# Kernel tuning notes

Hardware: AMD Instinct MI355X
Metric: run time of the kernel (lower is better)

The kernel has to match this reference:

```python
import jax, jax.numpy as jnp
import numpy as np

B, N, C = 4, 2048, 1024
H = 16
D = C // H
FF = 4096
EPS = 1e-6


def _layernorm(x, g, b):
    mu = jnp.mean(x, axis=-1, keepdims=True)
    var = jnp.mean(jnp.square(x - mu), axis=-1, keepdims=True)
    return (x - mu) * jax.lax.rsqrt(var + EPS) * g + b


def setup_inputs() -> dict:
    key = jax.random.key(0)
    ks = jax.random.split(key, 8)
    s = 0.02
    x = jax.random.normal(ks[0], (B, N, C), dtype=jnp.float32)
    mask = jnp.tril(jnp.ones((N, N), dtype=bool))[None, None]  # causal [1,1,N,N]
    return {
        "x": x,
        "mask": mask,
        "qkv_w": jax.random.normal(ks[1], (3 * C, C), jnp.float32) * s,
        "qkv_b": jnp.zeros((3 * C,), jnp.float32),
        "proj_w": jax.random.normal(ks[2], (C, C), jnp.float32) * s,
        "proj_b": jnp.zeros((C,), jnp.float32),
        "ln1_g": jnp.ones((C,), jnp.float32),
        "ln1_b": jnp.zeros((C,), jnp.float32),
        "ln2_g": jnp.ones((C,), jnp.float32),
        "ln2_b": jnp.zeros((C,), jnp.float32),
        "w1": jax.random.normal(ks[3], (FF, C), jnp.float32) * s,
        "w2": jax.random.normal(ks[4], (C, FF), jnp.float32) * s,
        "w3": jax.random.normal(ks[5], (FF, C), jnp.float32) * s,
    }


def reference(x, mask, qkv_w, qkv_b, proj_w, proj_b, ln1_g, ln1_b, ln2_g, ln2_b, w1, w2, w3):
    # --- attention sub-block (pre-norm) ---
    h = _layernorm(x, ln1_g, ln1_b)
    qkv = h @ qkv_w.T + qkv_b                      # [B,N,3C]
    qkv = qkv.reshape(B, N, 3, H, D).transpose(2, 0, 3, 1, 4)  # [3,B,H,N,D]
    q, k, v = qkv[0], qkv[1], qkv[2]
    scale = D ** -0.5
    attn = jnp.einsum("bhnd,bhmd->bhnm", q, k) * scale
    attn = jnp.where(mask, attn, -jnp.inf)
    attn = jax.nn.softmax(attn, axis=-1)
    o = jnp.einsum("bhnm,bhmd->bhnd", attn, v)
    o = o.transpose(0, 2, 1, 3).reshape(B, N, C)
    o = o @ proj_w.T + proj_b
    x = x + o  # dropout is identity in eval mode
    # --- SwiGLU MLP sub-block (pre-norm) ---
    h = _layernorm(x, ln2_g, ln2_b)
    m = (jax.nn.silu(h @ w1.T) * (h @ w3.T)) @ w2.T
    return x + m
```

## Files before the change

kernel.cpp:

```cpp
#include <hip/hip_runtime.h>
#include <hip/hip_bf16.h>
#include <stdint.h>

#define NB   4
#define NSEQ 2048
#define NC   1024
#define NH   16
#define ND   64
#define NFF  4096
#define NM   (NB*NSEQ)

typedef __attribute__((ext_vector_type(8))) short short8v;
typedef __attribute__((ext_vector_type(4))) short short4v;
typedef __attribute__((ext_vector_type(4))) float f32x4;

#define GPTR(p) ((const __attribute__((address_space(1))) void*)(p))
#define LPTR(p) ((__attribute__((address_space(3))) void*)(p))

__device__ __forceinline__ short f2bf(float f){
  unsigned u = __builtin_bit_cast(unsigned, f);
  u += 0x7fffu + ((u >> 16) & 1u);
  return (short)(u >> 16);
}
__device__ __forceinline__ float bf2f(short h){
  unsigned u = ((unsigned)(unsigned short)h) << 16;
  return __builtin_bit_cast(float, u);
}
__device__ __forceinline__ f32x4 mfma16x32(short8v a, short8v b, f32x4 c){
  return __builtin_amdgcn_mfma_f32_16x16x32_bf16(a, b, c, 0, 0, 0);
}
__device__ __forceinline__ f32x4 mfma16x16(short4v a, short4v b, f32x4 c){
  return __builtin_amdgcn_mfma_f32_16x16x16bf16_1k(a, b, c, 0, 0, 0);
}
__device__ __forceinline__ short4v pack4bf(f32x4 v){
  __hip_bfloat162 a = __float22bfloat162_rn(float2{v[0], v[1]});
  __hip_bfloat162 b = __float22bfloat162_rn(float2{v[2], v[3]});
  short4v r;
  __builtin_memcpy(&r, &a, 4);
  __builtin_memcpy(((char*)&r) + 4, &b, 4);
  return r;
}

__device__ __forceinline__ int xcd_swizzle(){
  int nwg = gridDim.x * gridDim.y;
  int wg  = blockIdx.y * gridDim.x + blockIdx.x;
  return (wg & 7) * (nwg >> 3) + (wg >> 3);
}

__global__ __launch_bounds__(256) void cvt_kernel(const float* __restrict__ w,
                                                  short* __restrict__ o, int n){
  int i = (blockIdx.x * 256 + threadIdx.x) * 4;
  if (i >= n) return;
  float4 v = *(const float4*)(w + i);
  short4v r = { f2bf(v.x), f2bf(v.y), f2bf(v.z), f2bf(v.w) };
  *(short4v*)(o + i) = r;
}

__global__ __launch_bounds__(256) void ln_kernel(const float* __restrict__ x,
                                                 const float* __restrict__ g,
                                                 const float* __restrict__ bta,
                                                 short* __restrict__ out){
  int row = blockIdx.x;
  int tid = threadIdx.x;
  int lane = tid & 63, w = tid >> 6;
  const float4* xr = (const float4*)(x + (size_t)row * NC);
  float4 v = xr[tid];
  float s1 = v.x + v.y + v.z + v.w;
  float s2 = v.x*v.x + v.y*v.y + v.z*v.z + v.w*v.w;
  #pragma unroll
  for (int off = 32; off; off >>= 1){
    s1 += __shfl_xor(s1, off);
    s2 += __shfl_xor(s2, off);
  }
  __shared__ float red[8];
  if (lane == 0){ red[w] = s1; red[4 + w] = s2; }
  __syncthreads();
  s1 = red[0] + red[1] + red[2] + red[3];
  s2 = red[4] + red[5] + red[6] + red[7];
  float mean = s1 * (1.0f / NC);
  float var  = s2 * (1.0f / NC) - mean * mean;
  float inv  = rsqrtf(var + 1e-6f);
  float4 gv = ((const float4*)g)[tid];
  float4 bv = ((const float4*)bta)[tid];
  short4v o = { f2bf((v.x - mean) * inv * gv.x + bv.x),
                f2bf((v.y - mean) * inv * gv.y + bv.y),
                f2bf((v.z - mean) * inv * gv.z + bv.z),
                f2bf((v.w - mean) * inv * gv.w + bv.w) };
  *(short4v*)(out + (size_t)row * NC + tid * 4) = o;
}

template<bool HAS_BIAS, bool HAS_RES, bool OUT_BF16, bool QKV_V>
__global__ __launch_bounds__(256, 2) void gemm_bt(const short* __restrict__ A,
                                                  const short* __restrict__ Bm,
                                                  const float* __restrict__ bias,
                                                  const float* __restrict__ res,
                                                  void* __restrict__ outp,
                                                  short* __restrict__ vt,
                                                  int Nc, int K){
  __shared__ short Al[128 * 32];
  __shared__ short Bl[128 * 32];
  int tid = threadIdx.x;
  int swz = xcd_swizzle();
  int m0 = (swz / gridDim.x) * 128, n0 = (swz % gridDim.x) * 128;
  const short* Ag = A + (size_t)m0 * K;
  const short* Bg = Bm + (size_t)n0 * K;
  int lr = tid >> 2, lc = (tid & 3) * 8;
  int lane = tid & 63, wid = tid >> 6;
  int wm = (wid >> 1) * 64, wn = (wid & 1) * 64;
  int qd = lane >> 4, l15 = lane & 15;

  f32x4 acc[4][4] = {};

  for (int k0 = 0; k0 < K; k0 += 32){
    __syncthreads();
    #pragma unroll
    for (int i = 0; i < 2; i++){
      int r = i * 64 + lr;
      __builtin_amdgcn_global_load_lds(GPTR(Ag + (size_t)r * K + k0 + lc),
                                       LPTR(&Al[r * 32 + lc]), 16, 0, 0);
      __builtin_amdgcn_global_load_lds(GPTR(Bg + (size_t)r * K + k0 + lc),
                                       LPTR(&Bl[r * 32 + lc]), 16, 0, 0);
    }
    __syncthreads();
    short8v a[4], b[4];
    #pragma unroll
    for (int t = 0; t < 4; t++)
      a[t] = *(const short8v*)&Al[(wm + t * 16 + l15) * 32 + qd * 8];
    #pragma unroll
    for (int t = 0; t < 4; t++)
      b[t] = *(const short8v*)&Bl[(wn + t * 16 + l15) * 32 + qd * 8];
    #pragma unroll
    for (int i = 0; i < 4; i++)
      #pragma unroll
      for (int j = 0; j < 4; j++)
        acc[i][j] = mfma16x32(a[i], b[j], acc[i][j]);
  }

  #pragma unroll
  for (int ti = 0; ti < 4; ti++){
    #pragma unroll
    for (int tj = 0; tj < 4; tj++){
      int col = n0 + wn + tj * 16 + l15;
      float bv = HAS_BIAS ? bias[col] : 0.0f;
      #pragma unroll
      for (int r = 0; r < 4; r++){
        int row = m0 + wm + ti * 16 + qd * 4 + r;
        float v = acc[ti][tj][r] + bv;
        if (QKV_V && col >= 2048){
          int hh = (col - 2048) >> 6, dd = col & 63;
          int bb = row >> 11, nn = row & 2047;
          vt[(((size_t)(bb * 16 + hh) * 64 + dd) << 11) + nn] = f2bf(v);
        } else {
          size_t idx = (size_t)row * Nc + col;
          if (HAS_RES) v += res[idx];
          if (OUT_BF16) ((short*)outp)[idx] = f2bf(v);
          else          ((float*)outp)[idx] = v;
        }
      }
    }
  }
}

__global__ __launch_bounds__(256, 2) void gemm_ff13(const short* __restrict__ A,
                                                    const short* __restrict__ B1m,
                                                    const short* __restrict__ B3m,
                                                    short* __restrict__ outp){
  __shared__ short Al [128 * 32];
  __shared__ short B1l[128 * 32];
  __shared__ short B3l[128 * 32];
  int tid = threadIdx.x;
  int swz = xcd_swizzle();
  int m0 = (swz / gridDim.x) * 128, n0 = (swz % gridDim.x) * 128;
  const short* Ag  = A   + (size_t)m0 * NC;
  const short* B1g = B1m + (size_t)n0 * NC;
  const short* B3g = B3m + (size_t)n0 * NC;
  int lr = tid >> 2, lc = (tid & 3) * 8;
  int lane = tid & 63, wid = tid >> 6;
  int wm = (wid >> 1) * 64, wn = (wid & 1) * 64;
  int qd = lane >> 4, l15 = lane & 15;

  f32x4 acc1[4][4] = {}, acc3[4][4] = {};

  for (int k0 = 0; k0 < NC; k0 += 32){
    __syncthreads();
    #pragma unroll
    for (int i = 0; i < 2; i++){
      int r = i * 64 + lr;
      __builtin_amdgcn_global_load_lds(GPTR(Ag + (size_t)r * NC + k0 + lc),
                                       LPTR(&Al[r * 32 + lc]), 16, 0, 0);
      __builtin_amdgcn_global_load_lds(GPTR(B1g + (size_t)r * NC + k0 + lc),
                                       LPTR(&B1l[r * 32 + lc]), 16, 0, 0);
      __builtin_amdgcn_global_load_lds(GPTR(B3g + (size_t)r * NC + k0 + lc),
                                       LPTR(&B3l[r * 32 + lc]), 16, 0, 0);
    }
    __syncthreads();
    short8v a[4], b1[4], b3[4];
    #pragma unroll
    for (int t = 0; t < 4; t++)
      a[t] = *(const short8v*)&Al[(wm + t * 16 + l15) * 32 + qd * 8];
    #pragma unroll
    for (int t = 0; t < 4; t++){
      b1[t] = *(const short8v*)&B1l[(wn + t * 16 + l15) * 32 + qd * 8];
      b3[t] = *(const short8v*)&B3l[(wn + t * 16 + l15) * 32 + qd * 8];
    }
    #pragma unroll
    for (int i = 0; i < 4; i++)
      #pragma unroll
      for (int j = 0; j < 4; j++){
        acc1[i][j] = mfma16x32(a[i], b1[j], acc1[i][j]);
        acc3[i][j] = mfma16x32(a[i], b3[j], acc3[i][j]);
      }
  }

  #pragma unroll
  for (int ti = 0; ti < 4; ti++){
    #pragma unroll
    for (int tj = 0; tj < 4; tj++){
      int col = n0 + wn + tj * 16 + l15;
      #pragma unroll
      for (int r = 0; r < 4; r++){
        int row = m0 + wm + ti * 16 + qd * 4 + r;
        float v1 = acc1[ti][tj][r];
        float v3 = acc3[ti][tj][r];
        float s = v1 / (1.0f + __expf(-v1)) * v3;
        outp[(size_t)row * NFF + col] = f2bf(s);
      }
    }
  }
}

__global__ __launch_bounds__(256) void attn_kernel(const short* __restrict__ qkvb,
                                                   const short* __restrict__ vt,
                                                   short* __restrict__ outb){
  const float QSCALE = 0.125f * 1.44269504f;
  int bh = blockIdx.x;
  int qb = 15 - blockIdx.y;
  int b = bh >> 4, h = bh & 15;
  int tid = threadIdx.x;
  int lane = tid & 63, wid = tid >> 6;
  int qd = lane >> 4, l15 = lane & 15;
  int qs = qb * 128 + wid * 32;

  const short* qbase = qkvb + (size_t)b * NSEQ * 3072 + h * 64;
  const short* kbase = qbase + 1024;
  const short* vtb   = vt + ((size_t)bh << 17);

  __shared__ short Kl[2][64 * 64];
  __shared__ short Vl[2][64 * 64];

  short8v qf[2][2];
  #pragma unroll
  for (int g = 0; g < 2; g++)
    #pragma unroll
    for (int kc = 0; kc < 2; kc++){
      short8v q = *(const short8v*)(qbase + (size_t)(qs + g * 16 + l15) * 3072
                                    + kc * 32 + qd * 8);
      short8v r;
      #pragma unroll
      for (int j = 0; j < 8; j++) r[j] = f2bf(bf2f(q[j]) * QSCALE);
      qf[g][kc] = r;
    }

  float l_i[2] = { 0.f, 0.f };
  f32x4 o[2][4];
  #pragma unroll
  for (int g = 0; g < 2; g++)
    #pragma unroll
    for (int t = 0; t < 4; t++)
      o[g][t] = (f32x4){0.f, 0.f, 0.f, 0.f};

  int nkt_blk = 2 * qb + 2;
  int itmax   = (qs + 31) >> 6;

  auto STAGE = [&](int bufi, int k0){
    #pragma unroll
    for (int i = 0; i < 2; i++){
      int cg = (wid * 2 + i) * 64 + lane;
      int r  = cg >> 3, c = cg & 7;
      int sc = (c ^ (r & 7)) << 3;
      __builtin_amdgcn_global_load_lds(GPTR(kbase + (size_t)(k0 + r) * 3072 + sc),
                                       LPTR(&Kl[bufi][cg * 8]), 16, 0, 0);
      __builtin_amdgcn_global_load_lds(GPTR(vtb + ((size_t)r << 11) + k0 + sc),
                                       LPTR(&Vl[bufi][cg * 8]), 16, 0, 0);
    }
  };

  STAGE(0, 0);
  __syncthreads();
  int cur = 0;

  for (int it = 0; it < nkt_blk; ++it){
    if (it + 1 < nkt_blk) STAGE(cur ^ 1, (it + 1) * 64);

    if (it <= itmax){
      int k0 = it * 64;
      short8v kf[4][2];
      #pragma unroll
      for (int kt = 0; kt < 4; kt++)
        #pragma unroll
        for (int kc = 0; kc < 2; kc++){
          int r = kt * 16 + l15;
          kf[kt][kc] = *(const short8v*)
              &Kl[cur][r * 64 + (((kc * 4 + qd) ^ (r & 7)) << 3)];
        }
      short4v vf[4][4];
      #pragma unroll
      for (int t = 0; t < 4; t++)
        #pragma unroll
        for (int ks = 0; ks < 4; ks++){
          int r = t * 16 + l15;
          vf[t][ks] = *(const short4v*)
              &Vl[cur][r * 64 + (((ks * 2 + (qd >> 1)) ^ (r & 7)) << 3)
                       + ((qd & 1) << 2)];
        }

      f32x4 s[2][4];
      #pragma unroll
      for (int g = 0; g < 2; g++)
        #pragma unroll
        for (int kt = 0; kt < 4; kt++){
          f32x4 z = (f32x4){0.f, 0.f, 0.f, 0.f};
          z = mfma16x32(kf[kt][0], qf[g][0], z);
          s[g][kt] = mfma16x32(kf[kt][1], qf[g][1], z);
        }

      if (it == itmax){
        #pragma unroll
        for (int g = 0; g < 2; g++){
          int qg = qs + g * 16 + l15;
          #pragma unroll
          for (int kt = 0; kt < 4; kt++)
            #pragma unroll
            for (int r = 0; r < 4; r++){
              int kg = k0 + kt * 16 + qd * 4 + r;
              s[g][kt][r] = (kg <= qg) ? s[g][kt][r] : -1e30f;
            }
        }
      }

      short4v pb[2][4];
      #pragma unroll
      for (int g = 0; g < 2; g++){
        #pragma unroll
        for (int kt = 0; kt < 4; kt++){
          f32x4 p;
          #pragma unroll
          for (int r = 0; r < 4; r++){
            float pv = exp2f(fminf(s[g][kt][r], 24.0f));
            p[r] = pv;
            l_i[g] += pv;
          }
          pb[g][kt] = pack4bf(p);
        }
      }

      #pragma unroll
      for (int g = 0; g < 2; g++)
        #pragma unroll
        for (int t = 0; t < 4; t++)
          #pragma unroll
          for (int ks = 0; ks < 4; ks++)
            o[g][t] = mfma16x16(vf[t][ks], pb[g][ks], o[g][t]);
    }

    __syncthreads();
    cur ^= 1;
  }

  #pragma unroll
  for (int g = 0; g < 2; g++){
    float l = l_i[g];
    l += __shfl_xor(l, 16);
    l += __shfl_xor(l, 32);
    float inv_l = 1.0f / l;
    int q = qs + g * 16 + l15;
    size_t rowbase = ((size_t)(b * NSEQ + q)) * NC + h * 64;
    #pragma unroll
    for (int t = 0; t < 4; t++){
      f32x4 v = { o[g][t][0] * inv_l, o[g][t][1] * inv_l,
                  o[g][t][2] * inv_l, o[g][t][3] * inv_l };
      *(short4v*)(outb + rowbase + t * 16 + qd * 4) = pack4bf(v);
    }
  }
}

extern "C" void kernel_launch(void* const* d_in, const int* in_sizes, int n_in,
                              void* d_out, int out_size, void* d_ws, size_t ws_size,
                              hipStream_t stream){
  const float* x      = (const float*)d_in[0];
  const float* qkv_w  = (const float*)d_in[2];
  const float* qkv_b  = (const float*)d_in[3];
  const float* proj_w = (const float*)d_in[4];
  const float* proj_b = (const float*)d_in[5];
  const float* ln1_g  = (const float*)d_in[6];
  const float* ln1_b  = (const float*)d_in[7];
  const float* ln2_g  = (const float*)d_in[8];
  const float* ln2_b  = (const float*)d_in[9];
  const float* w1     = (const float*)d_in[10];
  const float* w2     = (const float*)d_in[11];
  const float* w3     = (const float*)d_in[12];
  float* out = (float*)d_out;

  short* wqkv  = (short*)d_ws;
  short* wproj = wqkv  + (size_t)3072 * 1024;
  short* w1b   = wproj + (size_t)1024 * 1024;
  short* w3b   = w1b   + (size_t)4096 * 1024;
  short* w2b   = w3b   + (size_t)4096 * 1024;
  short* hb    = w2b   + (size_t)4096 * 1024;
  short* qkvb  = hb    + (size_t)NM * NC;
  short* attnb = qkvb  + (size_t)NM * 3072;
  short* ff3b  = attnb + (size_t)NM * NC;
  float* x1    = (float*)(ff3b + (size_t)NM * NFF);
  short* ff1b  = qkvb;
  short* vtb   = ff3b;

  cvt_kernel<<<3072 * 1024 / 1024, 256, 0, stream>>>(qkv_w, wqkv, 3072 * 1024);
  cvt_kernel<<<1024, 256, 0, stream>>>(proj_w, wproj, 1024 * 1024);
  cvt_kernel<<<4096, 256, 0, stream>>>(w1, w1b, 4096 * 1024);
  cvt_kernel<<<4096, 256, 0, stream>>>(w3, w3b, 4096 * 1024);
  cvt_kernel<<<4096, 256, 0, stream>>>(w2, w2b, 4096 * 1024);

  ln_kernel<<<NM, 256, 0, stream>>>(x, ln1_g, ln1_b, hb);
  gemm_bt<true, false, true, true><<<dim3(3072 / 128, NM / 128), 256, 0, stream>>>(
      hb, wqkv, qkv_b, nullptr, qkvb, vtb, 3072, 1024);
  attn_kernel<<<dim3(NB * NH, NSEQ / 128), 256, 0, stream>>>(qkvb, vtb, attnb);
  gemm_bt<true, true, false, false><<<dim3(1024 / 128, NM / 128), 256, 0, stream>>>(
      attnb, wproj, proj_b, x, x1, nullptr, 1024, 1024);
  ln_kernel<<<NM, 256, 0, stream>>>(x1, ln2_g, ln2_b, hb);
  gemm_ff13<<<dim3(4096 / 128, NM / 128), 256, 0, stream>>>(hb, w1b, w3b, ff1b);
  gemm_bt<false, true, false, false><<<dim3(1024 / 128, NM / 128), 256, 0, stream>>>(
      ff1b, w2b, nullptr, x1, out, nullptr, 1024, 4096);
}
```

Baseline: 629.3 us.

## Double GEMM K-tile to 64 with XOR-swizzled LDS and new ff13 block mapping

Both bf16 GEMM kernels now stage a 64-wide K slice per iteration instead of 32. This halves the number of barrier pairs per K loop. LDS rows are stored with an XOR swizzle of the 16-byte chunk index so the short8 fragment reads avoid bank conflicts. The generic GEMM's launch bound is raised to 3 blocks per CU, and the ff13 kernel remaps workgroups so each XCD owns a contiguous band of N columns for better weight reuse in L2. The larger LDS footprint (32-48 KB per block) may limit occupancy.

New measurement: 554.1 us. 12.0% less time.

```diff
diff --git a/kernel.cpp b/kernel.cpp
--- a/kernel.cpp
+++ b/kernel.cpp
@@ -39,12 +39,6 @@
   __builtin_memcpy(&r, &a, 4);
   __builtin_memcpy(((char*)&r) + 4, &b, 4);
   return r;
-}
-
-__device__ __forceinline__ int xcd_swizzle(){
-  int nwg = gridDim.x * gridDim.y;
-  int wg  = blockIdx.y * gridDim.x + blockIdx.x;
-  return (wg & 7) * (nwg >> 3) + (wg >> 3);
 }
 
 __global__ __launch_bounds__(256) void cvt_kernel(const float* __restrict__ w,
@@ -90,50 +84,60 @@
 }
 
 template<bool HAS_BIAS, bool HAS_RES, bool OUT_BF16, bool QKV_V>
-__global__ __launch_bounds__(256, 2) void gemm_bt(const short* __restrict__ A,
+__global__ __launch_bounds__(256, 3) void gemm_bt(const short* __restrict__ A,
                                                   const short* __restrict__ Bm,
                                                   const float* __restrict__ bias,
                                                   const float* __restrict__ res,
                                                   void* __restrict__ outp,
                                                   short* __restrict__ vt,
                                                   int Nc, int K){
-  __shared__ short Al[128 * 32];
-  __shared__ short Bl[128 * 32];
+  __shared__ short Al[128 * 64];
+  __shared__ short Bl[128 * 64];
   int tid = threadIdx.x;
-  int swz = xcd_swizzle();
-  int m0 = (swz / gridDim.x) * 128, n0 = (swz % gridDim.x) * 128;
+  int gx = gridDim.x, nwg = gx * gridDim.y;
+  int wg = blockIdx.y * gx + blockIdx.x;
+  int swz = (wg & 7) * (nwg >> 3) + (wg >> 3);
+  int m0 = (swz / gx) * 128, n0 = (swz % gx) * 128;
   const short* Ag = A + (size_t)m0 * K;
   const short* Bg = Bm + (size_t)n0 * K;
-  int lr = tid >> 2, lc = (tid & 3) * 8;
   int lane = tid & 63, wid = tid >> 6;
   int wm = (wid >> 1) * 64, wn = (wid & 1) * 64;
   int qd = lane >> 4, l15 = lane & 15;
 
   f32x4 acc[4][4] = {};
 
-  for (int k0 = 0; k0 < K; k0 += 32){
+  for (int k0 = 0; k0 < K; k0 += 64){
     __syncthreads();
     #pragma unroll
-    for (int i = 0; i < 2; i++){
-      int r = i * 64 + lr;
-      __builtin_amdgcn_global_load_lds(GPTR(Ag + (size_t)r * K + k0 + lc),
-                                       LPTR(&Al[r * 32 + lc]), 16, 0, 0);
-      __builtin_amdgcn_global_load_lds(GPTR(Bg + (size_t)r * K + k0 + lc),
-                                       LPTR(&Bl[r * 32 + lc]), 16, 0, 0);
+    for (int i = 0; i < 4; i++){
+      int cg = (wid * 4 + i) * 64 + lane;
+      int r  = cg >> 3, c = cg & 7;
+      int sc = (c ^ (r & 7)) << 3;
+      __builtin_amdgcn_global_load_lds(GPTR(Ag + (size_t)r * K + k0 + sc),
+                                       LPTR(&Al[cg * 8]), 16, 0, 0);
+      __builtin_amdgcn_global_load_lds(GPTR(Bg + (size_t)r * K + k0 + sc),
+                                       LPTR(&Bl[cg * 8]), 16, 0, 0);
     }
     __syncthreads();
-    short8v a[4], b[4];
-    #pragma unroll
-    for (int t = 0; t < 4; t++)
-      a[t] = *(const short8v*)&Al[(wm + t * 16 + l15) * 32 + qd * 8];
-    #pragma unroll
-    for (int t = 0; t < 4; t++)
-      b[t] = *(const short8v*)&Bl[(wn + t * 16 + l15) * 32 + qd * 8];
-    #pragma unroll
-    for (int i = 0; i < 4; i++)
-      #pragma unroll
-      for (int j = 0; j < 4; j++)
-        acc[i][j] = mfma16x32(a[i], b[j], acc[i][j]);
+    #pragma unroll
+    for (int kk = 0; kk < 2; kk++){
+      short8v a[4], b[4];
+      #pragma unroll
+      for (int t = 0; t < 4; t++){
+        int r = wm + t * 16 + l15;
+        a[t] = *(const short8v*)&Al[r * 64 + (((kk * 4 + qd) ^ (r & 7)) << 3)];
+      }
+      #pragma unroll
+      for (int t = 0; t < 4; t++){
+        int r = wn + t * 16 + l15;
+        b[t] = *(const short8v*)&Bl[r * 64 + (((kk * 4 + qd) ^ (r & 7)) << 3)];
+      }
+      #pragma unroll
+      for (int i = 0; i < 4; i++)
+        #pragma unroll
+        for (int j = 0; j < 4; j++)
+          acc[i][j] = mfma16x32(a[i], b[j], acc[i][j]);
+    }
   }
 
   #pragma unroll
@@ -165,51 +169,63 @@
                                                     const short* __restrict__ B1m,
                                                     const short* __restrict__ B3m,
                                                     short* __restrict__ outp){
-  __shared__ short Al [128 * 32];
-  __shared__ short B1l[128 * 32];
-  __shared__ short B3l[128 * 32];
+  __shared__ short Al [128 * 64];
+  __shared__ short B1l[128 * 64];
+  __shared__ short B3l[128 * 64];
   int tid = threadIdx.x;
-  int swz = xcd_swizzle();
-  int m0 = (swz / gridDim.x) * 128, n0 = (swz % gridDim.x) * 128;
+  int gx = gridDim.x;
+  int wg = blockIdx.y * gx + blockIdx.x;
+  int xcd = wg & 7, idx = wg >> 3;
+  int npx = gx >> 3;
+  int n0 = (xcd * npx + idx % npx) * 128;
+  int m0 = (idx / npx) * 128;
   const short* Ag  = A   + (size_t)m0 * NC;
   const short* B1g = B1m + (size_t)n0 * NC;
   const short* B3g = B3m + (size_t)n0 * NC;
-  int lr = tid >> 2, lc = (tid & 3) * 8;
   int lane = tid & 63, wid = tid >> 6;
   int wm = (wid >> 1) * 64, wn = (wid & 1) * 64;
   int qd = lane >> 4, l15 = lane & 15;
 
   f32x4 acc1[4][4] = {}, acc3[4][4] = {};
 
-  for (int k0 = 0; k0 < NC; k0 += 32){
+  for (int k0 = 0; k0 < NC; k0 += 64){
     __syncthreads();
     #pragma unroll
-    for (int i = 0; i < 2; i++){
-      int r = i * 64 + lr;
-      __builtin_amdgcn_global_load_lds(GPTR(Ag + (size_t)r * NC + k0 + lc),
-                                       LPTR(&Al[r * 32 + lc]), 16, 0, 0);
-      __builtin_amdgcn_global_load_lds(GPTR(B1g + (size_t)r * NC + k0 + lc),
-                                       LPTR(&B1l[r * 32 + lc]), 16, 0, 0);
-      __builtin_amdgcn_global_load_lds(GPTR(B3g + (size_t)r * NC + k0 + lc),
-                                       LPTR(&B3l[r * 32 + lc]), 16, 0, 0);
+    for (int i = 0; i < 4; i++){
+      int cg = (wid * 4 + i) * 64 + lane;
+      int r  = cg >> 3, c = cg & 7;
+      int sc = (c ^ (r & 7)) << 3;
+      __builtin_amdgcn_global_load_lds(GPTR(Ag + (size_t)r * NC + k0 + sc),
+                                       LPTR(&Al[cg * 8]), 16, 0, 0);
+      __builtin_amdgcn_global_load_lds(GPTR(B1g + (size_t)r * NC + k0 + sc),
+                                       LPTR(&B1l[cg * 8]), 16, 0, 0);
+      __builtin_amdgcn_global_load_lds(GPTR(B3g + (size_t)r * NC + k0 + sc),
+                                       LPTR(&B3l[cg * 8]), 16, 0, 0);
     }
     __syncthreads();
-    short8v a[4], b1[4], b3[4];
-    #pragma unroll
-    for (int t = 0; t < 4; t++)
-      a[t] = *(const short8v*)&Al[(wm + t * 16 + l15) * 32 + qd * 8];
-    #pragma unroll
-    for (int t = 0; t < 4; t++){
-      b1[t] = *(const short8v*)&B1l[(wn + t * 16 + l15) * 32 + qd * 8];
-      b3[t] = *(const short8v*)&B3l[(wn + t * 16 + l15) * 32 + qd * 8];
-    }
-    #pragma unroll
-    for (int i = 0; i < 4; i++)
-      #pragma unroll
-      for (int j = 0; j < 4; j++){
-        acc1[i][j] = mfma16x32(a[i], b1[j], acc1[i][j]);
-        acc3[i][j] = mfma16x32(a[i], b3[j], acc3[i][j]);
-      }
+    #pragma unroll
+    for (int kk = 0; kk < 2; kk++){
+      short8v a[4], b1[4], b3[4];
+      #pragma unroll
+      for (int t = 0; t < 4; t++){
+        int r = wm + t * 16 + l15;
+        a[t] = *(const short8v*)&Al[r * 64 + (((kk * 4 + qd) ^ (r & 7)) << 3)];
+      }
+      #pragma unroll
+      for (int t = 0; t < 4; t++){
+        int r = wn + t * 16 + l15;
+        int co = ((kk * 4 + qd) ^ (r & 7)) << 3;
+        b1[t] = *(const short8v*)&B1l[r * 64 + co];
+        b3[t] = *(const short8v*)&B3l[r * 64 + co];
+      }
+      #pragma unroll
+      for (int i = 0; i < 4; i++)
+        #pragma unroll
+        for (int j = 0; j < 4; j++){
+          acc1[i][j] = mfma16x32(a[i], b1[j], acc1[i][j]);
+          acc3[i][j] = mfma16x32(a[i], b3[j], acc3[i][j]);
+        }
+    }
   }
 
   #pragma unroll
```
